# Kernel tuning notes

Hardware: AMD Instinct MI355X
Metric: run time of the kernel (lower is better)

Reference implementation:

```python
import jax, jax.numpy as jnp
import numpy as np
import math

DIM = 2048
N_HEADS = 16
N_KV_HEADS = 8
HEAD_DIM = DIM // N_HEADS  # 128
N_REP = N_HEADS // N_KV_HEADS  # 2
SEQ = 2048
BATCH = 1
HIDDEN = 5632  # round_up(int(2*(4*2048)/3), 256)
NORM_EPS = 1e-5
LN_EPS = 1e-5  # torch.nn.LayerNorm default
ROPE_THETA = 10000.0


def rmsnorm(x, w, eps=NORM_EPS):
    x32 = x.astype(jnp.float32)
    n = x32 * jax.lax.rsqrt(jnp.mean(x32 * x32, axis=-1, keepdims=True) + eps)
    return n.astype(x.dtype) * w


def layernorm(x, w, b, eps=LN_EPS):
    mu = jnp.mean(x, axis=-1, keepdims=True)
    var = jnp.mean((x - mu) ** 2, axis=-1, keepdims=True)
    return (x - mu) * jax.lax.rsqrt(var + eps) * w + b


def apply_rope(x, cos, sin):
    # x: [B,S,H,hd]; cos/sin: [S, hd//2] -> complex multiply on (even, odd) pairs
    xr = x.reshape(*x.shape[:-1], HEAD_DIM // 2, 2)
    x0, x1 = xr[..., 0], xr[..., 1]
    c = cos[None, :, None, :]
    s = sin[None, :, None, :]
    o0 = x0 * c - x1 * s
    o1 = x0 * s + x1 * c
    return jnp.stack([o0, o1], axis=-1).reshape(x.shape)


def setup_inputs() -> dict:
    key = jax.random.key(0)
    ks = jax.random.split(key, 10)
    scale = 0.02
    x = jax.random.normal(ks[0], (BATCH, SEQ, DIM), jnp.float32)
    # RoPE tables
    inv_freq = 1.0 / (ROPE_THETA ** (jnp.arange(0, HEAD_DIM, 2, dtype=jnp.float32) / HEAD_DIM))
    ang = jnp.arange(SEQ, dtype=jnp.float32)[:, None] * inv_freq[None, :]  # [S, hd//2]
    freqs_cos = jnp.cos(ang)
    freqs_sin = jnp.sin(ang)
    # causal additive mask
    mask = jnp.where(jnp.tril(jnp.ones((SEQ, SEQ), bool)), 0.0, -1e9).astype(jnp.float32)
    wqkv = jax.random.normal(ks[1], ((N_HEADS + 2 * N_KV_HEADS) * HEAD_DIM, DIM), jnp.float32) * scale
    wo = jax.random.normal(ks[2], (DIM, N_HEADS * HEAD_DIM), jnp.float32) * scale
    qn_w = jnp.ones((HEAD_DIM,), jnp.float32)
    qn_b = jnp.zeros((HEAD_DIM,), jnp.float32)
    kn_w = jnp.ones((HEAD_DIM,), jnp.float32)
    kn_b = jnp.zeros((HEAD_DIM,), jnp.float32)
    attn_norm_w = jnp.ones((DIM,), jnp.float32)
    ffn_norm_w = jnp.ones((DIM,), jnp.float32)
    w13 = jax.random.normal(ks[3], (2 * HIDDEN, DIM), jnp.float32) * scale
    w2 = jax.random.normal(ks[4], (DIM, HIDDEN), jnp.float32) * scale
    return dict(x=x, freqs_cos=freqs_cos, freqs_sin=freqs_sin, mask=mask,
                wqkv=wqkv, wo=wo, qn_w=qn_w, qn_b=qn_b, kn_w=kn_w, kn_b=kn_b,
                attn_norm_w=attn_norm_w, ffn_norm_w=ffn_norm_w, w13=w13, w2=w2)


def reference(x, freqs_cos, freqs_sin, mask, wqkv, wo, qn_w, qn_b, kn_w, kn_b,
              attn_norm_w, ffn_norm_w, w13, w2):
    B, S, _ = x.shape
    # ---- attention sublayer (pre-norm) ----
    h = rmsnorm(x, attn_norm_w)
    qkv = h @ wqkv.T  # [B,S,(H+2KV)*hd]
    q_sz = N_HEADS * HEAD_DIM
    kv_sz = N_KV_HEADS * HEAD_DIM
    q = qkv[..., :q_sz].reshape(B, S, N_HEADS, HEAD_DIM)
    k = qkv[..., q_sz:q_sz + kv_sz].reshape(B, S, N_KV_HEADS, HEAD_DIM)
    v = qkv[..., q_sz + kv_sz:].reshape(B, S, N_KV_HEADS, HEAD_DIM)
    # QK-LayerNorm (per head_dim)
    q = layernorm(q, qn_w, qn_b)
    k = layernorm(k, kn_w, kn_b)
    # RoPE
    q = apply_rope(q, freqs_cos, freqs_sin)
    k = apply_rope(k, freqs_cos, freqs_sin)
    # GQA: repeat kv heads (interleaved like torch repeat_interleave on head dim)
    k = jnp.repeat(k, N_REP, axis=2)
    v = jnp.repeat(v, N_REP, axis=2)
    # scores with fp32 softmax
    scores = jnp.einsum('bqhd,bkhd->bhqk', q, k) / math.sqrt(HEAD_DIM)
    scores = scores + mask[None, None, :, :]
    p = jax.nn.softmax(scores.astype(jnp.float32), axis=-1).astype(q.dtype)
    o = jnp.einsum('bhqk,bkhd->bqhd', p, v).reshape(B, S, N_HEADS * HEAD_DIM)
    attn_out = o @ wo.T
    h = x + attn_out
    # ---- SwiGLU FFN sublayer ----
    g = rmsnorm(h, ffn_norm_w)
    x13 = g @ w13.T
    x1, x3 = x13[..., :HIDDEN], x13[..., HIDDEN:]
    out = h + (jax.nn.silu(x1) * x3) @ w2.T
    return out
```

## Files before the change

kernel.cpp:

```cpp
#include <hip/hip_runtime.h>
#include <math.h>

#define DIM 2048
#define SEQ 2048
#define NH 16
#define NKV 8
#define HD 128
#define HIDDEN 5632
#define QKV_N 4096
#define FF_N 11264

typedef __attribute__((ext_vector_type(8))) short s16x8;
typedef __attribute__((ext_vector_type(4))) float f32x4;

#define GPTR(p) ((const __attribute__((address_space(1))) void*)(p))
#define LPTR(p) ((__attribute__((address_space(3))) void*)(p))

#define CFENCE() __asm__ __volatile__("" ::: "memory")
#define BAR() do { CFENCE(); __builtin_amdgcn_s_barrier(); CFENCE(); } while (0)

__device__ __forceinline__ unsigned short f2bf(float f) {
    union { float f; unsigned u; } v; v.f = f;
    unsigned r = v.u + 0x7fff + ((v.u >> 16) & 1);
    return (unsigned short)(r >> 16);
}
__device__ __forceinline__ float bf2f(unsigned short s) {
    union { unsigned u; float f; } v; v.u = ((unsigned)s) << 16;
    return v.f;
}

__global__ __launch_bounds__(256) void k_cvt(const float* __restrict__ src,
                                             unsigned short* __restrict__ dst, int n4) {
    int i = blockIdx.x * 256 + threadIdx.x;
    if (i < n4) {
        float4 v = ((const float4*)src)[i];
        ushort4 o;
        o.x = f2bf(v.x); o.y = f2bf(v.y); o.z = f2bf(v.z); o.w = f2bf(v.w);
        ((ushort4*)dst)[i] = o;
    }
}

__global__ __launch_bounds__(256) void k_rmsnorm(const float* __restrict__ x,
                                                 const float* __restrict__ w,
                                                 unsigned short* __restrict__ out) {
    int row = blockIdx.x;
    int tid = threadIdx.x, wv = tid >> 6, lane = tid & 63;
    const float* xr = x + (size_t)row * DIM;
    float4 a = ((const float4*)xr)[tid * 2];
    float4 b = ((const float4*)xr)[tid * 2 + 1];
    float ss = a.x*a.x + a.y*a.y + a.z*a.z + a.w*a.w
             + b.x*b.x + b.y*b.y + b.z*b.z + b.w*b.w;
    for (int off = 32; off >= 1; off >>= 1) ss += __shfl_xor(ss, off);
    __shared__ float red[4];
    if (lane == 0) red[wv] = ss;
    __syncthreads();
    float tot = red[0] + red[1] + red[2] + red[3];
    float rs = rsqrtf(tot * (1.0f / DIM) + 1e-5f);
    float4 wa = ((const float4*)w)[tid * 2];
    float4 wb = ((const float4*)w)[tid * 2 + 1];
    ushort4 o0, o1;
    o0.x = f2bf(a.x * rs * wa.x); o0.y = f2bf(a.y * rs * wa.y);
    o0.z = f2bf(a.z * rs * wa.z); o0.w = f2bf(a.w * rs * wa.w);
    o1.x = f2bf(b.x * rs * wb.x); o1.y = f2bf(b.y * rs * wb.y);
    o1.z = f2bf(b.z * rs * wb.z); o1.w = f2bf(b.w * rs * wb.w);
    ushort4* orow = (ushort4*)(out + (size_t)row * DIM);
    orow[tid * 2] = o0; orow[tid * 2 + 1] = o1;
}

template<int ID>
__global__ __launch_bounds__(512, 2) void k_gemm256(
    const unsigned short* __restrict__ A, const unsigned short* __restrict__ B,
    int M, int N, int K, int Kslice,
    float* __restrict__ Cf, unsigned short* __restrict__ Cb,
    const float* __restrict__ add, int flags) {
    __shared__ __align__(16) unsigned short As[2][16384];
    __shared__ __align__(16) unsigned short Bs[2][16384];
    int tid = threadIdx.x;
    int wv = tid >> 6, lane = tid & 63, quad = lane >> 4, l15 = lane & 15;
    int wr = wv >> 2, wc = wv & 3;
    int rowBase = blockIdx.y * 256;
    int colBase = blockIdx.x * 256;
    int kb = blockIdx.z * Kslice;
    int NT = Kslice >> 6;

    f32x4 acc[8][4] = {};

    auto stageA = [&](int t, int kh, int b) {
#pragma unroll
        for (int j = 0; j < 2; j++) {
            int u = j * 8 + wv;
            int kg = u >> 2;
            int m0 = (u & 3) * 64;
            const unsigned short* g = A + (size_t)(rowBase + m0 + lane) * K
                                        + (kb + t * 64 + kh * 32 + kg * 8);
            __builtin_amdgcn_global_load_lds(GPTR(g),
                LPTR(&As[b][((kh * 4 + kg) * 256 + m0) * 8]), 16, 0, 0);
        }
    };
    auto stageB = [&](int t, int kh, int b) {
#pragma unroll
        for (int j = 0; j < 2; j++) {
            int u = j * 8 + wv;
            int kg = u >> 2;
            int m0 = (u & 3) * 64;
            const unsigned short* g = B + (size_t)(colBase + m0 + lane) * K
                                        + (kb + t * 64 + kh * 32 + kg * 8);
            __builtin_amdgcn_global_load_lds(GPTR(g),
                LPTR(&Bs[b][((kh * 4 + kg) * 256 + m0) * 8]), 16, 0, 0);
        }
    };

    stageA(0, 0, 0); stageB(0, 0, 0); stageB(0, 1, 0); stageA(0, 1, 0);
    if (NT > 1) {
        stageA(1, 0, 1); stageB(1, 0, 1); stageB(1, 1, 1);
        asm volatile("s_waitcnt vmcnt(6)" ::: "memory");
    } else {
        asm volatile("s_waitcnt vmcnt(0)" ::: "memory");
    }
    BAR();

    for (int T = 0; T < NT; T++) {
        const int b = T & 1;
        s16x8 a0[8], a1[8], b0[4], b1[4];
#pragma unroll
        for (int mt = 0; mt < 8; mt++)
            a0[mt] = *(const s16x8*)&As[b][(quad * 256 + wr * 128 + mt * 16 + l15) * 8];
#pragma unroll
        for (int nt = 0; nt < 4; nt++)
            b0[nt] = *(const s16x8*)&Bs[b][(quad * 256 + wc * 64 + nt * 16 + l15) * 8];
        if (T + 1 < NT) stageA(T + 1, 1, b ^ 1);
        BAR();
        asm volatile("s_waitcnt lgkmcnt(0)" ::: "memory");
        __builtin_amdgcn_s_setprio(1);
#pragma unroll
        for (int mt = 0; mt < 8; mt++) {
            acc[mt][0] = __builtin_amdgcn_mfma_f32_16x16x32_bf16(a0[mt], b0[0], acc[mt][0], 0, 0, 0);
            acc[mt][1] = __builtin_amdgcn_mfma_f32_16x16x32_bf16(a0[mt], b0[1], acc[mt][1], 0, 0, 0);
        }
        __builtin_amdgcn_s_setprio(0);
        BAR();
#pragma unroll
        for (int nt = 0; nt < 4; nt++)
            b1[nt] = *(const s16x8*)&Bs[b][((4 + quad) * 256 + wc * 64 + nt * 16 + l15) * 8];
        if (T + 2 < NT) stageA(T + 2, 0, b);
        BAR();
        asm volatile("s_waitcnt lgkmcnt(0)" ::: "memory");
        __builtin_amdgcn_s_setprio(1);
#pragma unroll
        for (int mt = 0; mt < 8; mt++) {
            acc[mt][2] = __builtin_amdgcn_mfma_f32_16x16x32_bf16(a0[mt], b0[2], acc[mt][2], 0, 0, 0);
            acc[mt][3] = __builtin_amdgcn_mfma_f32_16x16x32_bf16(a0[mt], b0[3], acc[mt][3], 0, 0, 0);
        }
        __builtin_amdgcn_s_setprio(0);
        BAR();
#pragma unroll
        for (int mt = 0; mt < 8; mt++)
            a1[mt] = *(const s16x8*)&As[b][((4 + quad) * 256 + wr * 128 + mt * 16 + l15) * 8];
        if (T + 2 < NT) stageB(T + 2, 0, b);
        BAR();
        asm volatile("s_waitcnt lgkmcnt(0)" ::: "memory");
        __builtin_amdgcn_s_setprio(1);
#pragma unroll
        for (int mt = 0; mt < 8; mt++) {
            acc[mt][0] = __builtin_amdgcn_mfma_f32_16x16x32_bf16(a1[mt], b1[0], acc[mt][0], 0, 0, 0);
            acc[mt][1] = __builtin_amdgcn_mfma_f32_16x16x32_bf16(a1[mt], b1[1], acc[mt][1], 0, 0, 0);
        }
        __builtin_amdgcn_s_setprio(0);
        BAR();
        if (T + 2 < NT) stageB(T + 2, 1, b);
        BAR();
        __builtin_amdgcn_s_setprio(1);
#pragma unroll
        for (int mt = 0; mt < 8; mt++) {
            acc[mt][2] = __builtin_amdgcn_mfma_f32_16x16x32_bf16(a1[mt], b1[2], acc[mt][2], 0, 0, 0);
            acc[mt][3] = __builtin_amdgcn_mfma_f32_16x16x32_bf16(a1[mt], b1[3], acc[mt][3], 0, 0, 0);
        }
        __builtin_amdgcn_s_setprio(0);
        if (T + 2 < NT) asm volatile("s_waitcnt vmcnt(6)" ::: "memory");
        else            asm volatile("s_waitcnt vmcnt(0)" ::: "memory");
        BAR();
    }

    float* Cfz = Cf ? Cf + (size_t)blockIdx.z * M * N : nullptr;
#pragma unroll
    for (int mt = 0; mt < 8; mt++)
#pragma unroll
        for (int nt = 0; nt < 4; nt++)
#pragma unroll
            for (int r = 0; r < 4; r++) {
                int row = rowBase + wr * 128 + mt * 16 + quad * 4 + r;
                int col = colBase + wc * 64 + nt * 16 + l15;
                size_t idx = (size_t)row * N + col;
                float v = acc[mt][nt][r];
                if (flags == 1) v += add[idx];
                if (flags == 2) Cb[idx] = f2bf(v);
                else            Cfz[idx] = v;
            }
}

__global__ __launch_bounds__(256) void k_red5(const float* __restrict__ p,
                                              size_t pstride,
                                              const float* __restrict__ res,
                                              float* __restrict__ o, int n4) {
    int i = blockIdx.x * 256 + threadIdx.x;
    if (i < n4) {
        float4 r = ((const float4*)res)[i];
#pragma unroll
        for (int z = 0; z < 4; z++) {
            float4 v = ((const float4*)(p + z * pstride))[i];
            r.x += v.x; r.y += v.y; r.z += v.z; r.w += v.w;
        }
        ((float4*)o)[i] = r;
    }
}

__global__ __launch_bounds__(256) void k_qknorm_rope(
    const float* __restrict__ qkv,
    const float* __restrict__ qw, const float* __restrict__ qb,
    const float* __restrict__ kw, const float* __restrict__ kb,
    const float* __restrict__ fcos, const float* __restrict__ fsin,
    unsigned short* __restrict__ qout, unsigned short* __restrict__ kfrag) {
    int wv = threadIdx.x >> 6, lane = threadIdx.x & 63;
    int hl = blockIdx.y;
    int s = blockIdx.x * 4 + wv;
    bool isq = hl < 16;
    float2 xv = *(const float2*)&qkv[(size_t)s * QKV_N + hl * HD + 2 * lane];
    float sum = xv.x + xv.y, ssq = xv.x * xv.x + xv.y * xv.y;
    for (int off = 32; off >= 1; off >>= 1) {
        sum += __shfl_xor(sum, off);
        ssq += __shfl_xor(ssq, off);
    }
    float mu = sum * (1.0f / HD);
    float var = ssq * (1.0f / HD) - mu * mu;
    float rs = rsqrtf(var + 1e-5f);
    const float* w_ = isq ? qw : kw;
    const float* b_ = isq ? qb : kb;
    float n0 = (xv.x - mu) * rs * w_[2 * lane]     + b_[2 * lane];
    float n1 = (xv.y - mu) * rs * w_[2 * lane + 1] + b_[2 * lane + 1];
    float c = fcos[s * 64 + lane], sn = fsin[s * 64 + lane];
    float o0 = n0 * c - n1 * sn;
    float o1 = n0 * sn + n1 * c;
    if (isq) {
        const float sc = 0.12751744f;
        o0 *= sc; o1 *= sc;
        unsigned val = (unsigned)f2bf(o0) | ((unsigned)f2bf(o1) << 16);
        *(unsigned*)&qout[((size_t)hl * SEQ + s) * HD + 2 * lane] = val;
    } else {
        int kvh = hl - 16;
        int kt = s >> 6, key = s & 63;
        int dg = lane >> 2, j = (2 * lane) & 7;
        unsigned val = (unsigned)f2bf(o0) | ((unsigned)f2bf(o1) << 16);
        size_t idx = (((size_t)(kvh * 32 + kt) * 16 + dg) * 64 + key) * 8 + j;
        *(unsigned*)&kfrag[idx] = val;
    }
}

__global__ __launch_bounds__(256) void k_vprep(const float* __restrict__ qkv,
                                               unsigned short* __restrict__ vfrag) {
    __shared__ unsigned short lv[64][132];
    int kvh = blockIdx.y, kt = blockIdx.x, tid = threadIdx.x;
#pragma unroll
    for (int it = 0; it < 8; it++) {
        int li = it * 256 + tid;
        int row = li >> 5;
        int c4 = (li & 31) * 4;
        float4 v = *(const float4*)&qkv[(size_t)(kt * 64 + row) * QKV_N + 3072 + kvh * HD + c4];
        lv[row][c4] = f2bf(v.x); lv[row][c4 + 1] = f2bf(v.y);
        lv[row][c4 + 2] = f2bf(v.z); lv[row][c4 + 3] = f2bf(v.w);
    }
    __syncthreads();
    size_t base = (size_t)(kvh * 32 + kt) * 8192;
#pragma unroll
    for (int it = 0; it < 16; it++) {
        int o2 = it * 256 + tid;
        int e = o2 * 2;
        int r = e & 7, d = (e >> 3) & 127, kg = e >> 10;
        unsigned val = (unsigned)lv[kg * 8 + r][d] | ((unsigned)lv[kg * 8 + r + 1][d] << 16);
        *(unsigned*)&vfrag[base + e] = val;
    }
}

__global__ __launch_bounds__(256) void k_flash(
    const unsigned short* __restrict__ q,
    const unsigned short* __restrict__ kfrag,
    const unsigned short* __restrict__ vfrag,
    unsigned short* __restrict__ o) {
    __shared__ __align__(16) unsigned short Ks[2][8192];
    __shared__ __align__(16) unsigned short Vs[2][8192];
    __shared__ __align__(16) unsigned short Ps[4][16 * 72];
    int h = blockIdx.x & 15;
    int qt = 31 - (blockIdx.x >> 4);
    int kvh = h >> 1;
    int tid = threadIdx.x, wv = tid >> 6, lane = tid & 63, quad = lane >> 4, l15 = lane & 15;
    int qbase = qt * 64;

    s16x8 qf[4];
    {
        const unsigned short* qp = q + ((size_t)h * SEQ + qbase + wv * 16 + l15) * HD + quad * 8;
#pragma unroll
        for (int ks = 0; ks < 4; ks++) qf[ks] = *(const s16x8*)(qp + ks * 32);
    }
    f32x4 oacc[8] = {};
    float mst[4], lst[4];
#pragma unroll
    for (int r = 0; r < 4; r++) { mst[r] = -3e38f; lst[r] = 0.f; }

    auto issueKV = [&](int kt, int b) {
        size_t kb = (size_t)(kvh * 32 + kt) * 8192;
#pragma unroll
        for (int i = 0; i < 4; i++) {
            int s0 = i * 256 + wv * 64;
            __builtin_amdgcn_global_load_lds(GPTR(kfrag + kb + (size_t)(s0 + lane) * 8), LPTR(&Ks[b][s0 * 8]), 16, 0, 0);
            __builtin_amdgcn_global_load_lds(GPTR(vfrag + kb + (size_t)(s0 + lane) * 8), LPTR(&Vs[b][s0 * 8]), 16, 0, 0);
        }
    };

    issueKV(0, 0);
    for (int kt = 0; kt <= qt; kt++) {
        int b = kt & 1;
        __syncthreads();
        if (kt < qt) issueKV(kt + 1, b ^ 1);

        f32x4 sacc[4];
#pragma unroll
        for (int nt = 0; nt < 4; nt++) {
            f32x4 a = {};
#pragma unroll
            for (int ks = 0; ks < 4; ks++) {
                s16x8 kf = *(const s16x8*)&Ks[b][((ks * 4 + quad) * 64 + nt * 16 + l15) * 8];
                a = __builtin_amdgcn_mfma_f32_16x16x32_bf16(qf[ks], kf, a, 0, 0, 0);
            }
            sacc[nt] = a;
        }
        if (kt == qt) {
#pragma unroll
            for (int nt = 0; nt < 4; nt++) {
                int colg = kt * 64 + nt * 16 + l15;
#pragma unroll
                for (int r = 0; r < 4; r++) {
                    int rowg = qbase + wv * 16 + quad * 4 + r;
                    if (colg > rowg) sacc[nt][r] = -3e38f;
                }
            }
        }
        unsigned short* Pw = Ps[wv];
#pragma unroll
        for (int r = 0; r < 4; r++) {
            float mx = fmaxf(fmaxf(sacc[0][r], sacc[1][r]), fmaxf(sacc[2][r], sacc[3][r]));
#pragma unroll
            for (int off = 1; off < 16; off <<= 1) mx = fmaxf(mx, __shfl_xor(mx, off));
            float mnew = fmaxf(mst[r], mx);
            float alpha = exp2f(mst[r] - mnew);
            float psum = 0.f;
#pragma unroll
            for (int nt = 0; nt < 4; nt++) {
                float p = exp2f(sacc[nt][r] - mnew);
                psum += p;
                Pw[(quad * 4 + r) * 72 + nt * 16 + l15] = f2bf(p);
            }
#pragma unroll
            for (int off = 1; off < 16; off <<= 1) psum += __shfl_xor(psum, off);
            lst[r] = lst[r] * alpha + psum;
            mst[r] = mnew;
#pragma unroll
            for (int vt = 0; vt < 8; vt++) oacc[vt][r] *= alpha;
        }
#pragma unroll
        for (int ks = 0; ks < 2; ks++) {
            s16x8 pf = *(const s16x8*)&Pw[l15 * 72 + ks * 32 + quad * 8];
#pragma unroll
            for (int vt = 0; vt < 8; vt++) {
                s16x8 vf = *(const s16x8*)&Vs[b][((ks * 4 + quad) * 128 + vt * 16 + l15) * 8];
                oacc[vt] = __builtin_amdgcn_mfma_f32_16x16x32_bf16(pf, vf, oacc[vt], 0, 0, 0);
            }
        }
    }
#pragma unroll
    for (int r = 0; r < 4; r++) {
        float inv = 1.0f / lst[r];
        int row = qbase + wv * 16 + quad * 4 + r;
#pragma unroll
        for (int vt = 0; vt < 8; vt++)
            o[(size_t)row * DIM + h * HD + vt * 16 + l15] = f2bf(oacc[vt][r] * inv);
    }
}

__global__ __launch_bounds__(256) void k_silu(const unsigned short* __restrict__ x13,
                                              unsigned short* __restrict__ y) {
    int gid = blockIdx.x * 256 + threadIdx.x;
    int s = gid / 1408;
    int j4 = (gid - s * 1408) * 4;
    const unsigned short* p1 = x13 + (size_t)s * FF_N + j4;
    const unsigned short* p3 = p1 + HIDDEN;
    ushort4 a = *(const ushort4*)p1;
    ushort4 b = *(const ushort4*)p3;
    ushort4 o;
    {
        float x1 = bf2f(a.x), x3 = bf2f(b.x);
        o.x = f2bf(x1 / (1.f + __expf(-x1)) * x3);
    }
    {
        float x1 = bf2f(a.y), x3 = bf2f(b.y);
        o.y = f2bf(x1 / (1.f + __expf(-x1)) * x3);
    }
    {
        float x1 = bf2f(a.z), x3 = bf2f(b.z);
        o.z = f2bf(x1 / (1.f + __expf(-x1)) * x3);
    }
    {
        float x1 = bf2f(a.w), x3 = bf2f(b.w);
        o.w = f2bf(x1 / (1.f + __expf(-x1)) * x3);
    }
    *(ushort4*)&y[(size_t)s * HIDDEN + j4] = o;
}

extern "C" void kernel_launch(void* const* d_in, const int* in_sizes, int n_in,
                              void* d_out, int out_size, void* d_ws, size_t ws_size,
                              hipStream_t stream) {
    const float* x    = (const float*)d_in[0];
    const float* fcos = (const float*)d_in[1];
    const float* fsin = (const float*)d_in[2];
    const float* wqkv = (const float*)d_in[4];
    const float* wo   = (const float*)d_in[5];
    const float* qn_w = (const float*)d_in[6];
    const float* qn_b = (const float*)d_in[7];
    const float* kn_w = (const float*)d_in[8];
    const float* kn_b = (const float*)d_in[9];
    const float* anw  = (const float*)d_in[10];
    const float* fnw  = (const float*)d_in[11];
    const float* w13  = (const float*)d_in[12];
    const float* w2   = (const float*)d_in[13];
    float* out = (float*)d_out;
    char* ws = (char*)d_ws;

    size_t off = 0;
    auto alloc = [&](size_t bytes) { size_t o = off; off += (bytes + 255) & ~(size_t)255; return o; };
    unsigned short* wqkv_b = (unsigned short*)(ws + alloc((size_t)QKV_N * DIM * 2));
    unsigned short* wo_b   = (unsigned short*)(ws + alloc((size_t)DIM * DIM * 2));
    unsigned short* w13_b  = (unsigned short*)(ws + alloc((size_t)FF_N * DIM * 2));
    unsigned short* w2_b   = (unsigned short*)(ws + alloc((size_t)DIM * HIDDEN * 2));
    unsigned short* xn     = (unsigned short*)(ws + alloc((size_t)SEQ * DIM * 2));
    float*          qkv    = (float*)         (ws + alloc((size_t)SEQ * QKV_N * 4));
    unsigned short* qb_    = (unsigned short*)(ws + alloc((size_t)NH * SEQ * HD * 2));
    unsigned short* kfr    = (unsigned short*)(ws + alloc((size_t)NKV * SEQ * HD * 2));
    unsigned short* vfr    = (unsigned short*)(ws + alloc((size_t)NKV * SEQ * HD * 2));
    unsigned short* ob     = (unsigned short*)(ws + alloc((size_t)SEQ * DIM * 2));
    float*          hbuf   = (float*)         (ws + alloc((size_t)SEQ * DIM * 4));
    unsigned short* gb     = (unsigned short*)(ws + alloc((size_t)SEQ * DIM * 2));
    unsigned short* x13b   = (unsigned short*)(ws + alloc((size_t)SEQ * FF_N * 2));
    unsigned short* yb     = (unsigned short*)(ws + alloc((size_t)SEQ * HIDDEN * 2));
    float*          pp     = (float*)         (ws + alloc((size_t)4 * SEQ * DIM * 4));
    const size_t pstride = (size_t)SEQ * DIM;

    k_cvt<<<8192, 256, 0, stream>>>(wqkv, wqkv_b, QKV_N * DIM / 4);
    k_cvt<<<4096, 256, 0, stream>>>(wo, wo_b, DIM * DIM / 4);
    k_cvt<<<22528, 256, 0, stream>>>(w13, w13_b, FF_N * DIM / 4);
    k_cvt<<<11264, 256, 0, stream>>>(w2, w2_b, DIM * HIDDEN / 4);

    k_rmsnorm<<<SEQ, 256, 0, stream>>>(x, anw, xn);
    k_gemm256<0><<<dim3(QKV_N / 256, SEQ / 256), 512, 0, stream>>>(
        xn, wqkv_b, SEQ, QKV_N, DIM, DIM, qkv, nullptr, nullptr, 0);
    k_qknorm_rope<<<dim3(SEQ / 4, NH + NKV), 256, 0, stream>>>(
        qkv, qn_w, qn_b, kn_w, kn_b, fcos, fsin, qb_, kfr);
    k_vprep<<<dim3(SEQ / 64, NKV), 256, 0, stream>>>(qkv, vfr);
    k_flash<<<NH * (SEQ / 64), 256, 0, stream>>>(qb_, kfr, vfr, ob);
    k_gemm256<1><<<dim3(DIM / 256, SEQ / 256, 4), 512, 0, stream>>>(
        ob, wo_b, SEQ, DIM, DIM, DIM / 4, pp, nullptr, nullptr, 0);
    k_red5<<<SEQ * DIM / 1024, 256, 0, stream>>>(pp, pstride, x, hbuf, SEQ * DIM / 4);
    k_rmsnorm<<<SEQ, 256, 0, stream>>>(hbuf, fnw, gb);
    k_gemm256<2><<<dim3(FF_N / 256, SEQ / 256), 512, 0, stream>>>(
        gb, w13_b, SEQ, FF_N, DIM, DIM, nullptr, x13b, nullptr, 2);
    k_silu<<<SEQ * (HIDDEN / 4) / 256, 256, 0, stream>>>(x13b, yb);
    k_gemm256<3><<<dim3(DIM / 256, SEQ / 256, 4), 512, 0, stream>>>(
        yb, w2_b, SEQ, DIM, HIDDEN, HIDDEN / 4, pp, nullptr, nullptr, 0);
    k_red5<<<SEQ * DIM / 1024, 256, 0, stream>>>(pp, pstride, hbuf, out, SEQ * DIM / 4);
}
```

Measured before the change: 802.7 us.

## Switch GEMM LDS tiles to row-major XOR-swizzled layout and restage loads

Changes the shared-memory layout of the A and B tiles from k-group-major chunks to row-major 64-element rows with an XOR swizzle on the 16-byte chunk index. Global loads now fetch 8 contiguous chunks per row for coalescing, and fragment reads apply the matching swizzle to avoid bank conflicts. The prefetch schedule is also reorganised so B and A tiles for step T+2 are staged in whole halves at two later points, and the vmcnt wait threshold changes to match. The main risk is whether the new staging order and wait counts still keep buffer reuse correct while overlapping enough load latency.

```diff
diff --git a/kernel.cpp b/kernel.cpp
--- a/kernel.cpp
+++ b/kernel.cpp
@@ -85,35 +85,36 @@
 
     f32x4 acc[8][4] = {};
 
-    auto stageA = [&](int t, int kh, int b) {
+    int srow = lane >> 3;
+    int schunk = lane & 7;
+
+    auto stage = [&](const unsigned short* Mat, int matBase,
+                     unsigned short (*Ls)[16384], int t, int h, int b) {
 #pragma unroll
         for (int j = 0; j < 2; j++) {
-            int u = j * 8 + wv;
-            int kg = u >> 2;
-            int m0 = (u & 3) * 64;
-            const unsigned short* g = A + (size_t)(rowBase + m0 + lane) * K
-                                        + (kb + t * 64 + kh * 32 + kg * 8);
-            __builtin_amdgcn_global_load_lds(GPTR(g),
-                LPTR(&As[b][((kh * 4 + kg) * 256 + m0) * 8]), 16, 0, 0);
+            int r0 = h * 128 + (j * 8 + wv) * 8;
+            int row = r0 + srow;
+            int kchunk = schunk ^ (row & 7);
+            const unsigned short* g = Mat + (size_t)(matBase + row) * K
+                                      + (kb + t * 64 + kchunk * 8);
+            __builtin_amdgcn_global_load_lds(GPTR(g), LPTR(&Ls[b][r0 * 64]), 16, 0, 0);
         }
     };
-    auto stageB = [&](int t, int kh, int b) {
-#pragma unroll
-        for (int j = 0; j < 2; j++) {
-            int u = j * 8 + wv;
-            int kg = u >> 2;
-            int m0 = (u & 3) * 64;
-            const unsigned short* g = B + (size_t)(colBase + m0 + lane) * K
-                                        + (kb + t * 64 + kh * 32 + kg * 8);
-            __builtin_amdgcn_global_load_lds(GPTR(g),
-                LPTR(&Bs[b][((kh * 4 + kg) * 256 + m0) * 8]), 16, 0, 0);
-        }
+    auto LDA = [&](int b_, int mt, int ks) -> s16x8 {
+        int row = wr * 128 + mt * 16 + l15;
+        return *(const s16x8*)&As[b_][row * 64 + ((((ks * 4 + quad)) ^ (row & 7)) << 3)];
     };
-
-    stageA(0, 0, 0); stageB(0, 0, 0); stageB(0, 1, 0); stageA(0, 1, 0);
+    auto LDB = [&](int b_, int nt, int ks) -> s16x8 {
+        int row = wc * 64 + nt * 16 + l15;
+        return *(const s16x8*)&Bs[b_][row * 64 + ((((ks * 4 + quad)) ^ (row & 7)) << 3)];
+    };
+
+    stage(B, colBase, Bs, 0, 0, 0); stage(B, colBase, Bs, 0, 1, 0);
+    stage(A, rowBase, As, 0, 0, 0); stage(A, rowBase, As, 0, 1, 0);
     if (NT > 1) {
-        stageA(1, 0, 1); stageB(1, 0, 1); stageB(1, 1, 1);
-        asm volatile("s_waitcnt vmcnt(6)" ::: "memory");
+        stage(B, colBase, Bs, 1, 0, 1); stage(B, colBase, Bs, 1, 1, 1);
+        stage(A, rowBase, As, 1, 0, 1); stage(A, rowBase, As, 1, 1, 1);
+        asm volatile("s_waitcnt vmcnt(8)" ::: "memory");
     } else {
         asm volatile("s_waitcnt vmcnt(0)" ::: "memory");
     }
@@ -123,12 +124,9 @@
         const int b = T & 1;
         s16x8 a0[8], a1[8], b0[4], b1[4];
 #pragma unroll
-        for (int mt = 0; mt < 8; mt++)
-            a0[mt] = *(const s16x8*)&As[b][(quad * 256 + wr * 128 + mt * 16 + l15) * 8];
-#pragma unroll
-        for (int nt = 0; nt < 4; nt++)
-            b0[nt] = *(const s16x8*)&Bs[b][(quad * 256 + wc * 64 + nt * 16 + l15) * 8];
-        if (T + 1 < NT) stageA(T + 1, 1, b ^ 1);
+        for (int mt = 0; mt < 8; mt++) a0[mt] = LDA(b, mt, 0);
+#pragma unroll
+        for (int nt = 0; nt < 4; nt++) b0[nt] = LDB(b, nt, 0);
         BAR();
         asm volatile("s_waitcnt lgkmcnt(0)" ::: "memory");
         __builtin_amdgcn_s_setprio(1);
@@ -140,9 +138,7 @@
         __builtin_amdgcn_s_setprio(0);
         BAR();
 #pragma unroll
-        for (int nt = 0; nt < 4; nt++)
-            b1[nt] = *(const s16x8*)&Bs[b][((4 + quad) * 256 + wc * 64 + nt * 16 + l15) * 8];
-        if (T + 2 < NT) stageA(T + 2, 0, b);
+        for (int nt = 0; nt < 4; nt++) b1[nt] = LDB(b, nt, 1);
         BAR();
         asm volatile("s_waitcnt lgkmcnt(0)" ::: "memory");
         __builtin_amdgcn_s_setprio(1);
@@ -154,9 +150,8 @@
         __builtin_amdgcn_s_setprio(0);
         BAR();
 #pragma unroll
-        for (int mt = 0; mt < 8; mt++)
-            a1[mt] = *(const s16x8*)&As[b][((4 + quad) * 256 + wr * 128 + mt * 16 + l15) * 8];
-        if (T + 2 < NT) stageB(T + 2, 0, b);
+        for (int mt = 0; mt < 8; mt++) a1[mt] = LDA(b, mt, 1);
+        if (T + 2 < NT) { stage(B, colBase, Bs, T + 2, 0, b); stage(B, colBase, Bs, T + 2, 1, b); }
         BAR();
         asm volatile("s_waitcnt lgkmcnt(0)" ::: "memory");
         __builtin_amdgcn_s_setprio(1);
@@ -167,7 +162,7 @@
         }
         __builtin_amdgcn_s_setprio(0);
         BAR();
-        if (T + 2 < NT) stageB(T + 2, 1, b);
+        if (T + 2 < NT) { stage(A, rowBase, As, T + 2, 0, b); stage(A, rowBase, As, T + 2, 1, b); }
         BAR();
         __builtin_amdgcn_s_setprio(1);
 #pragma unroll
@@ -176,7 +171,7 @@
             acc[mt][3] = __builtin_amdgcn_mfma_f32_16x16x32_bf16(a1[mt], b1[3], acc[mt][3], 0, 0, 0);
         }
         __builtin_amdgcn_s_setprio(0);
-        if (T + 2 < NT) asm volatile("s_waitcnt vmcnt(6)" ::: "memory");
+        if (T + 2 < NT) asm volatile("s_waitcnt vmcnt(8)" ::: "memory");
         else            asm volatile("s_waitcnt vmcnt(0)" ::: "memory");
         BAR();
     }
```

New measurement: 747.4 us. 1.07x faster.
